# Performance work log

Hardware: AMD Instinct MI355X
Metric: run time of the kernel (lower is better)

## Reference

```python
import jax, jax.numpy as jnp
import numpy as np

N_CIRC, N_MIR, N_DIS = 100_000, 50_000, 25_000
IN_CH, HID, OUT = 128, 64, 64


def setup_inputs() -> dict:
    key = jax.random.key(0)
    ks = iter(jax.random.split(key, 64))

    def nrm(shape, scale):
        return jax.random.normal(next(ks), shape, jnp.float32) * scale

    def edges(n_src, n_dst, E):
        s = jax.random.randint(next(ks), (E,), 0, n_src, jnp.int32)
        d = jax.random.randint(next(ks), (E,), 0, n_dst, jnp.int32)
        return jnp.stack([s, d])  # [2, E]

    inp = dict(
        x_circ=nrm((N_CIRC, IN_CH), 1.0),
        x_mir=nrm((N_MIR, IN_CH), 1.0),
        x_dis=nrm((N_DIS, IN_CH), 1.0),
        e_cm=edges(N_CIRC, N_MIR, 500_000),
        e_md=edges(N_MIR, N_DIS, 250_000),
        e_cd=edges(N_CIRC, N_DIS, 250_000),
        e_mc=edges(N_MIR, N_CIRC, 500_000),
        e_dm=edges(N_DIS, N_MIR, 250_000),
        e_dc=edges(N_DIS, N_CIRC, 250_000),
        e_cc=edges(N_CIRC, N_CIRC, 500_000),
        e_mm=edges(N_MIR, N_MIR, 250_000),
        # stacked SAGEConv params: lin_l (with bias) and lin_r (no bias), per relation
        W1l=nrm((6, HID, IN_CH), 0.08), W1r=nrm((6, HID, IN_CH), 0.08), b1=jnp.zeros((6, HID), jnp.float32),
        W2l=nrm((6, HID, HID), 0.12), W2r=nrm((6, HID, HID), 0.12), b2=jnp.zeros((6, HID), jnp.float32),
        W3l=nrm((8, OUT, HID), 0.12), W3r=nrm((8, OUT, HID), 0.12), b3=jnp.zeros((8, OUT), jnp.float32),
    )
    return inp


def _sage(x_src, x_dst, ei, Wl, bl, Wr, n_dst):
    # PyG SAGEConv: out = lin_l(mean_j x_src[j]) + lin_r(x_dst); isolated dst -> 0 agg
    src, dst = ei[0], ei[1]
    msum = jax.ops.segment_sum(x_src[src], dst, num_segments=n_dst)
    cnt = jax.ops.segment_sum(jnp.ones(src.shape, x_src.dtype), dst, num_segments=n_dst)
    agg = msum / jnp.maximum(cnt, 1.0)[:, None]
    return agg @ Wl.T + bl + x_dst @ Wr.T


def _hetero_layer(xc, xm, xd, Wl, Wr, b, es, with_sim):
    e_cm, e_md, e_cd, e_mc, e_dm, e_dc, e_cc, e_mm = es
    o_cm = _sage(xc, xm, e_cm, Wl[0], b[0], Wr[0], N_MIR)
    o_md = _sage(xm, xd, e_md, Wl[1], b[1], Wr[1], N_DIS)
    o_cd = _sage(xc, xd, e_cd, Wl[2], b[2], Wr[2], N_DIS)
    o_mc = _sage(xm, xc, e_mc, Wl[3], b[3], Wr[3], N_CIRC)
    o_dm = _sage(xd, xm, e_dm, Wl[4], b[4], Wr[4], N_MIR)
    o_dc = _sage(xd, xc, e_dc, Wl[5], b[5], Wr[5], N_CIRC)
    if with_sim:
        o_cc = _sage(xc, xc, e_cc, Wl[6], b[6], Wr[6], N_CIRC)
        o_mm = _sage(xm, xm, e_mm, Wl[7], b[7], Wr[7], N_MIR)
        hc = (o_mc + o_dc + o_cc) / 3.0
        hm = (o_cm + o_dm + o_mm) / 3.0
    else:
        hc = (o_mc + o_dc) / 2.0
        hm = (o_cm + o_dm) / 2.0
    hd = (o_md + o_cd) / 2.0  # HeteroConv aggr='mean' across relations
    return hc, hm, hd


def _l2norm(x):
    n = jnp.sqrt(jnp.sum(x * x, axis=1, keepdims=True))
    return x / jnp.maximum(n, 1e-12)


def reference(x_circ, x_mir, x_dis, e_cm, e_md, e_cd, e_mc, e_dm, e_dc, e_cc, e_mm,
              W1l, W1r, b1, W2l, W2r, b2, W3l, W3r, b3):
    es = (e_cm, e_md, e_cd, e_mc, e_dm, e_dc, e_cc, e_mm)
    hc, hm, hd = _hetero_layer(x_circ, x_mir, x_dis, W1l, W1r, b1, es, False)
    hc, hm, hd = jax.nn.relu(hc), jax.nn.relu(hm), jax.nn.relu(hd)  # dropout = identity (eval)
    hc, hm, hd = _hetero_layer(hc, hm, hd, W2l, W2r, b2, es, False)
    hc, hm, hd = jax.nn.relu(hc), jax.nn.relu(hm), jax.nn.relu(hd)
    oc, om, od = _hetero_layer(hc, hm, hd, W3l, W3r, b3, es, True)
    return _l2norm(oc), _l2norm(om), _l2norm(od)
```

## Files before the change

### kernel.cpp

```cpp
#include <hip/hip_runtime.h>
#include <hip/hip_bf16.h>

#define DIV_UP(a,b) (((a)+(b)-1)/(b))

typedef __bf16 bf16x8 __attribute__((ext_vector_type(8)));
typedef float  f32x4  __attribute__((ext_vector_type(4)));

__global__ __launch_bounds__(256) void detect_dtype(const unsigned int* __restrict__ x,
                                                    int* __restrict__ flag) {
  __shared__ int cnt_s;
  if (threadIdx.x == 0) cnt_s = 0;
  __syncthreads();
  unsigned w = x[threadIdx.x];
  unsigned lo_exp = (w >> 7) & 0xFF;
  if (lo_exp >= 100 && lo_exp <= 140) atomicAdd(&cnt_s, 1);
  __syncthreads();
  if (threadIdx.x == 0) flag[0] = (cnt_s >= 128) ? 1 : 0;
}

template<int K>
__global__ __launch_bounds__(256) void gemm_mfma(
    const void* __restrict__ x, int xmode,
    const void* __restrict__ w, int woff, int wmode,
    const int* __restrict__ flagp, __hip_bfloat16* __restrict__ out, int n) {
  constexpr int KP = K + 8;
  __shared__ __bf16 xs[64 * KP];
  const bool xb = (xmode == 2) ? (*flagp != 0) : (xmode == 1);
  const bool wb = (wmode == 2) ? (*flagp != 0) : (wmode == 1);
  const int t = threadIdx.x;
  const int wv = t >> 6;
  const int L = t & 63;
  const int m = L & 15, q = L >> 4;
  const int row0 = blockIdx.x * 64;
  const int col = wv * 16 + m;

  bf16x8 bfr[K / 32];
  if (wb) {
    const __bf16* wh = (const __bf16*)w + woff;
#pragma unroll
    for (int ks = 0; ks < K / 32; ++ks)
      bfr[ks] = *(const bf16x8*)&wh[col * K + ks * 32 + q * 8];
  } else {
    const float* wf = (const float*)w + woff;
#pragma unroll
    for (int ks = 0; ks < K / 32; ++ks) {
      bf16x8 b;
#pragma unroll
      for (int j = 0; j < 8; ++j) b[j] = (__bf16)wf[col * K + ks * 32 + q * 8 + j];
      bfr[ks] = b;
    }
  }

  constexpr int CH = K / 8;
  if (xb) {
    const __bf16* xh = (const __bf16*)x;
    for (int idx = t; idx < 64 * CH; idx += 256) {
      int r = idx / CH, c = idx % CH;
      int gr = row0 + r; gr = (gr < n) ? gr : (n - 1);
      *(bf16x8*)&xs[r * KP + c * 8] = *(const bf16x8*)&xh[(size_t)gr * K + c * 8];
    }
  } else {
    const float* xf = (const float*)x;
    for (int idx = t; idx < 64 * CH; idx += 256) {
      int r = idx / CH, c = idx % CH;
      int gr = row0 + r; gr = (gr < n) ? gr : (n - 1);
      const float* src = &xf[(size_t)gr * K + c * 8];
      bf16x8 v;
#pragma unroll
      for (int j = 0; j < 8; ++j) v[j] = (__bf16)src[j];
      *(bf16x8*)&xs[r * KP + c * 8] = v;
    }
  }
  __syncthreads();

  f32x4 acc[4] = {};
#pragma unroll
  for (int ks = 0; ks < K / 32; ++ks) {
#pragma unroll
    for (int rt = 0; rt < 4; ++rt) {
      bf16x8 a = *(const bf16x8*)&xs[(rt * 16 + m) * KP + ks * 32 + q * 8];
      acc[rt] = __builtin_amdgcn_mfma_f32_16x16x32_bf16(a, bfr[ks], acc[rt], 0, 0, 0);
    }
  }

#pragma unroll
  for (int rt = 0; rt < 4; ++rt) {
#pragma unroll
    for (int i = 0; i < 4; ++i) {
      int gr = row0 + rt * 16 + q * 4 + i;
      if (gr < n) out[(size_t)gr * 64 + col] = __float2bfloat16(acc[rt][i]);
    }
  }
}

template<int K, int MODE, int NREL>
__global__ __launch_bounds__(256) void fused_agg(
    const void* __restrict__ xdst, int xmode,
    const int* __restrict__ flagp,
    const __hip_bfloat16* __restrict__ wrsum,
    const float* __restrict__ bias,
    const int* __restrict__ col,
    const int* __restrict__ rp0, const __hip_bfloat16* __restrict__ y0,
    const int* __restrict__ rp1, const __hip_bfloat16* __restrict__ y1,
    const int* __restrict__ rp2, const __hip_bfloat16* __restrict__ y2,
    float invR,
    void* __restrict__ outp, size_t obase, int n) {
  constexpr int CAP = 512;
  __shared__ float dbuf[16][68];
  __shared__ int rpl_s[NREL][17];
  __shared__ int cbuf[NREL][CAP];
  const bool xb = (xmode == 2) ? (*flagp != 0) : (xmode == 1);
  const int t = threadIdx.x;
  const int wv = t >> 6, L = t & 63;
  const int m = L & 15, q = L >> 4;
  const int row0 = blockIdx.x * 16;
  const int colc = wv * 16 + m;

  const int* rps[3] = {rp0, rp1, rp2};
  int hi16 = row0 + 16; hi16 = (hi16 < n) ? hi16 : n;
  int sj[NREL]; bool fit[NREL];
#pragma unroll
  for (int j = 0; j < NREL; ++j) {
    sj[j] = rps[j][row0];
    int span = rps[j][hi16] - sj[j];
    fit[j] = (span <= CAP);
    int lim = fit[j] ? span : 0;
    for (int i = t; i < lim; i += 256) cbuf[j][i] = col[sj[j] + i];
  }

  if (t < NREL * 17) {
    int j = t / 17, k = t - j * 17;
    const int* rp = (j == 0) ? rp0 : (j == 1) ? rp1 : rp2;
    int gi = row0 + k; gi = (gi < n) ? gi : n;
    rpl_s[j][k] = rp[gi];
  }

  const __bf16* wh = (const __bf16*)wrsum;
  bf16x8 bfr[K / 32];
#pragma unroll
  for (int ks = 0; ks < K / 32; ++ks)
    bfr[ks] = *(const bf16x8*)&wh[colc * K + ks * 32 + q * 8];

  int ar = row0 + m; ar = (ar < n) ? ar : (n - 1);
  f32x4 acc = {};
  if (xb) {
    const __bf16* xp = (const __bf16*)xdst;
#pragma unroll
    for (int ks = 0; ks < K / 32; ++ks) {
      bf16x8 a = *(const bf16x8*)&xp[(size_t)ar * K + ks * 32 + q * 8];
      acc = __builtin_amdgcn_mfma_f32_16x16x32_bf16(a, bfr[ks], acc, 0, 0, 0);
    }
  } else {
    const float* xp = (const float*)xdst;
#pragma unroll
    for (int ks = 0; ks < K / 32; ++ks) {
      bf16x8 a;
#pragma unroll
      for (int j = 0; j < 8; ++j) a[j] = (__bf16)xp[(size_t)ar * K + ks * 32 + q * 8 + j];
      acc = __builtin_amdgcn_mfma_f32_16x16x32_bf16(a, bfr[ks], acc, 0, 0, 0);
    }
  }
  float bc = bias[colc];
#pragma unroll
  for (int i = 0; i < 4; ++i) dbuf[q * 4 + i][colc] = acc[i] + bc;
  __syncthreads();

  const char* ys[3] = {(const char*)y0, (const char*)y1, (const char*)y2};
  const int jj = L & 31;
  const int half = L >> 5;
  const unsigned jb = (unsigned)jj << 2;

#pragma unroll 1
  for (int pass = 0; pass < 2; ++pass) {
    int b0[2][NREL], dg[2][NREL];
    float g0[2][NREL], g1[2][NREL];
    int nbmax = 0;
#pragma unroll
    for (int u = 0; u < 2; ++u) {
      const int lr = wv * 4 + pass * 2 + u;
#pragma unroll
      for (int j = 0; j < NREL; ++j) {
        int s = rpl_s[j][lr], e = rpl_s[j][lr + 1];
        b0[u][j] = s; dg[u][j] = e - s;
        g0[u][j] = 0.0f; g1[u][j] = 0.0f;
        int nbj = (e - s + 3) >> 2;
        nbmax = (nbj > nbmax) ? nbj : nbmax;
      }
    }

#pragma unroll 1
    for (int b = 0; b < nbmax; ++b) {
      const int bb = b << 2;
      unsigned wd[2][NREL][2];
#pragma unroll
      for (int u = 0; u < 2; ++u)
#pragma unroll
        for (int j = 0; j < NREL; ++j) {
          int rem = dg[u][j] - bb;
          if (rem > 0) {
            int last = rem - 1;
            int o0 = (half < last) ? half : last;
            int o1 = (2 + half < last) ? (2 + half) : last;
            unsigned c0, c1;
            if (fit[j]) {
              int lp = b0[u][j] - sj[j] + bb;
              c0 = (unsigned)cbuf[j][lp + o0];
              c1 = (unsigned)cbuf[j][lp + o1];
            } else {
              int p = b0[u][j] + bb;
              c0 = (unsigned)col[p + o0];
              c1 = (unsigned)col[p + o1];
            }
            wd[u][j][0] = *(const unsigned*)(ys[j] + ((c0 << 7) + jb));
            wd[u][j][1] = *(const unsigned*)(ys[j] + ((c1 << 7) + jb));
          }
        }
#pragma unroll
      for (int u = 0; u < 2; ++u)
#pragma unroll
        for (int j = 0; j < NREL; ++j) {
          int rem = dg[u][j] - bb;
          if (rem > 0) {
            unsigned w0 = (half < rem) ? wd[u][j][0] : 0u;
            unsigned w1 = (2 + half < rem) ? wd[u][j][1] : 0u;
            g0[u][j] += __uint_as_float(w0 << 16) + __uint_as_float(w1 << 16);
            g1[u][j] += __uint_as_float(w0 & 0xffff0000u) + __uint_as_float(w1 & 0xffff0000u);
          }
        }
    }

#pragma unroll
    for (int u = 0; u < 2; ++u) {
      const int lr = wv * 4 + pass * 2 + u;
      const int gr = row0 + lr;
      if (gr >= n) continue;
      float t0 = 0.0f, t1 = 0.0f;
#pragma unroll
      for (int j = 0; j < NREL; ++j) {
        float idg = (dg[u][j] > 0) ? (1.0f / (float)dg[u][j]) : 0.0f;
        t0 += g0[u][j] * idg; t1 += g1[u][j] * idg;
      }
      t0 += __shfl_xor(t0, 32, 64);
      t1 += __shfl_xor(t1, 32, 64);
      float2 d2 = *(const float2*)&dbuf[lr][2 * jj];
      float s0 = (d2.x + t0) * invR;
      float s1 = (d2.y + t1) * invR;

      if (MODE == 0) {
        if (half == 0) {
          __hip_bfloat16 b0v = __float2bfloat16(fmaxf(s0, 0.0f));
          __hip_bfloat16 b1v = __float2bfloat16(fmaxf(s1, 0.0f));
          unsigned pw = ((unsigned)*(const unsigned short*)&b1v << 16) |
                        (unsigned)*(const unsigned short*)&b0v;
          *(unsigned*)((__hip_bfloat16*)outp + obase + (size_t)gr * 64 + 2 * jj) = pw;
        }
      } else {
        float ss = s0 * s0 + s1 * s1;
#pragma unroll
        for (int o = 16; o > 0; o >>= 1) ss += __shfl_xor(ss, o, 64);
        float sc = 1.0f / fmaxf(sqrtf(ss), 1e-12f);
        float r0 = s0 * sc, r1 = s1 * sc;
        if (half == 0) {
          size_t idx = obase + (size_t)gr * 64 + 2 * jj;
          if (*flagp) {
            __hip_bfloat16 b0v = __float2bfloat16(r0);
            __hip_bfloat16 b1v = __float2bfloat16(r1);
            unsigned pw = ((unsigned)*(const unsigned short*)&b1v << 16) |
                          (unsigned)*(const unsigned short*)&b0v;
            *(unsigned*)((__hip_bfloat16*)outp + idx) = pw;
          } else {
            float2 v; v.x = r0; v.y = r1;
            *(float2*)((float*)outp + idx) = v;
          }
        }
      }
    }
  }
}

__global__ __launch_bounds__(256) void count_int(const int* __restrict__ ed,
                                                 int* __restrict__ deg, int E) {
  int i = blockIdx.x * 256 + threadIdx.x;
  if (i < E) atomicAdd(&deg[ed[i]], 1);
}

__global__ __launch_bounds__(256) void scan1(const int* __restrict__ deg,
    int* __restrict__ outp, int* __restrict__ part, int n) {
  __shared__ int tmp[256];
  int gid = blockIdx.x * 256 + threadIdx.x;
  int v = (gid < n) ? deg[gid] : 0;
  tmp[threadIdx.x] = v;
  __syncthreads();
  for (int off = 1; off < 256; off <<= 1) {
    int t = (threadIdx.x >= off) ? tmp[threadIdx.x - off] : 0;
    __syncthreads();
    tmp[threadIdx.x] += t;
    __syncthreads();
  }
  if (gid < n) outp[gid] = tmp[threadIdx.x] - v;
  if (threadIdx.x == 255) part[blockIdx.x] = tmp[255];
}

__global__ __launch_bounds__(256) void scan2(int* __restrict__ part, int P,
                                             int* __restrict__ totalout) {
  __shared__ int tmp[256];
  __shared__ int carry;
  if (threadIdx.x == 0) carry = 0;
  __syncthreads();
  for (int base0 = 0; base0 < P; base0 += 256) {
    int i = base0 + threadIdx.x;
    int v = (i < P) ? part[i] : 0;
    tmp[threadIdx.x] = v;
    __syncthreads();
    for (int off = 1; off < 256; off <<= 1) {
      int t = (threadIdx.x >= off) ? tmp[threadIdx.x - off] : 0;
      __syncthreads();
      tmp[threadIdx.x] += t;
      __syncthreads();
    }
    if (i < P) part[i] = tmp[threadIdx.x] - v + carry;
    __syncthreads();
    if (threadIdx.x == 0) carry += tmp[255];
    __syncthreads();
  }
  if (threadIdx.x == 0) *totalout = carry;
}

__global__ __launch_bounds__(256) void scan3(int* __restrict__ outp,
    const int* __restrict__ part, int n) {
  int gid = blockIdx.x * 256 + threadIdx.x;
  if (gid < n) outp[gid] += part[blockIdx.x];
}

__global__ __launch_bounds__(256) void copy_int(const int* __restrict__ src,
                                                int* __restrict__ dst, int n) {
  int i = blockIdx.x * 256 + threadIdx.x;
  if (i < n) dst[i] = src[i];
}

__global__ __launch_bounds__(256) void fill_csr(const int* __restrict__ es,
    const int* __restrict__ ed, int* __restrict__ cursor, int* __restrict__ col, int E) {
  int i = blockIdx.x * 256 + threadIdx.x;
  if (i < E) {
    int pos = atomicAdd(&cursor[ed[i]], 1);
    col[pos] = es[i];
  }
}

__global__ __launch_bounds__(256) void wsum_kernel(
    const void* __restrict__ W, int o0, int o1, int o2,
    const void* __restrict__ B, int p0, int p1, int p2,
    const int* __restrict__ flagp, __hip_bfloat16* __restrict__ wout,
    float* __restrict__ bout, int wsz) {
  const bool bf = (*flagp != 0);
  int i = blockIdx.x * 256 + threadIdx.x;
  float s = 0.0f, sb = 0.0f;
  if (bf) {
    const __hip_bfloat16* Wp = (const __hip_bfloat16*)W;
    const __hip_bfloat16* Bp = (const __hip_bfloat16*)B;
    if (i < wsz) {
      s = __bfloat162float(Wp[o0 + i]) + __bfloat162float(Wp[o1 + i]);
      if (o2 >= 0) s += __bfloat162float(Wp[o2 + i]);
    }
    if (i < 64) {
      sb = __bfloat162float(Bp[p0 + i]) + __bfloat162float(Bp[p1 + i]);
      if (p2 >= 0) sb += __bfloat162float(Bp[p2 + i]);
    }
  } else {
    const float* Wp = (const float*)W;
    const float* Bp = (const float*)B;
    if (i < wsz) {
      s = Wp[o0 + i] + Wp[o1 + i];
      if (o2 >= 0) s += Wp[o2 + i];
    }
    if (i < 64) {
      sb = Bp[p0 + i] + Bp[p1 + i];
      if (p2 >= 0) sb += Bp[p2 + i];
    }
  }
  if (i < wsz) wout[i] = __float2bfloat16(s);
  if (i < 64) bout[i] = sb;
}

extern "C" void kernel_launch(void* const* d_in, const int* in_sizes, int n_in,
                              void* d_out, int out_size, void* d_ws, size_t ws_size,
                              hipStream_t stream) {
  const int NC = 100000, NM = 50000, ND = 25000;
  const int nn[3] = {NC, NM, ND};
  const size_t toff[3] = {0, (size_t)NC * 64, (size_t)(NC + NM) * 64};
  const void* X[3] = {d_in[0], d_in[1], d_in[2]};
  const int* eptr[8]; int E[8];
  for (int r = 0; r < 8; ++r) { eptr[r] = (const int*)d_in[3 + r]; E[r] = in_sizes[3 + r] / 2; }
  const void* Wls[3] = {d_in[11], d_in[14], d_in[17]};
  const void* Wrs[3] = {d_in[12], d_in[15], d_in[18]};
  const void* Bbs[3] = {d_in[13], d_in[16], d_in[19]};

  const int src_t[8] = {0, 1, 0, 1, 2, 2, 0, 1};
  const int dst_t[8] = {1, 2, 2, 0, 1, 0, 0, 1};
  const int relT[3][3] = {{3, 5, 6}, {0, 4, 7}, {1, 2, -1}};

  int coff[8]; int cntN = 0;
  for (int r = 0; r < 8; ++r) { coff[r] = cntN; cntN += nn[dst_t[r]]; }
  int Etot = 0; for (int r = 0; r < 8; ++r) Etot += E[r];

  char* base = (char*)d_ws;
  auto carve = [&](size_t bytes) -> char* {
    char* p = (char*)(((uintptr_t)base + 127) & ~(uintptr_t)127);
    base = p + bytes;
    return p;
  };
  int* flag = (int*)carve(16);
  __hip_bfloat16* wr[3];
  for (int t = 0; t < 3; ++t) wr[t] = (__hip_bfloat16*)carve(64 * 128 * 2);
  float* bs[3]; for (int t = 0; t < 3; ++t) bs[t] = (float*)carve(64 * 4);
  __hip_bfloat16* y = (__hip_bfloat16*)carve((size_t)175000 * 64 * 2);
  int* degcur = (int*)carve((size_t)cntN * 4);
  int* rowptr = (int*)carve((size_t)(cntN + 1) * 4);
  int* part = (int*)carve((size_t)(DIV_UP(cntN, 256) + 1) * 4);
  int* col = (int*)carve((size_t)Etot * 4);
  __hip_bfloat16* h2 = (__hip_bfloat16*)carve((size_t)175000 * 64 * 2);
  __hip_bfloat16* h1 = (__hip_bfloat16*)d_out;
  (void)n_in; (void)out_size; (void)ws_size;

  detect_dtype<<<1, 256, 0, stream>>>((const unsigned int*)d_in[0], flag);

  hipMemsetAsync(degcur, 0, (size_t)cntN * sizeof(int), stream);
  for (int r = 0; r < 8; ++r)
    count_int<<<DIV_UP(E[r], 256), 256, 0, stream>>>(eptr[r] + E[r], degcur + coff[r], E[r]);
  int nb = DIV_UP(cntN, 256);
  scan1<<<nb, 256, 0, stream>>>(degcur, rowptr, part, cntN);
  scan2<<<1, 256, 0, stream>>>(part, nb, rowptr + cntN);
  scan3<<<nb, 256, 0, stream>>>(rowptr, part, cntN);
  copy_int<<<nb, 256, 0, stream>>>(rowptr, degcur, cntN);
  for (int r = 0; r < 8; ++r)
    fill_csr<<<DIV_UP(E[r], 256), 256, 0, stream>>>(eptr[r], eptr[r] + E[r],
                                                    degcur + coff[r], col, E[r]);

  for (int layer = 0; layer < 3; ++layer) {
    const void* Wl = Wls[layer];
    const void* Wr = Wrs[layer];
    const void* Bb = Bbs[layer];
    const int K = (layer == 0) ? 128 : 64;
    const int wsz = 64 * K;
    const __hip_bfloat16* hin = (layer == 1) ? h1 : h2;

    for (int T = 0; T < 3; ++T) {
      const int nrel = (layer == 2 && T < 2) ? 3 : 2;
      const int r0 = relT[T][0], r1 = relT[T][1];
      const int r2 = (nrel == 3) ? relT[T][2] : -1;
      wsum_kernel<<<DIV_UP(wsz, 256), 256, 0, stream>>>(
          Wr, r0 * wsz, r1 * wsz, (r2 >= 0) ? r2 * wsz : -1,
          Bb, r0 * 64, r1 * 64, (r2 >= 0) ? r2 * 64 : -1,
          flag, wr[T], bs[T], wsz);
      size_t yoffs[3] = {0, 0, 0};
      size_t yoff = 0;
      for (int j = 0; j < nrel; ++j) {
        int r = relT[T][j], st = src_t[r];
        yoffs[j] = yoff;
        if (layer == 0)
          gemm_mfma<128><<<DIV_UP(nn[st], 64), 256, 0, stream>>>(
              X[st], 2, Wl, r * wsz, 2, flag, y + yoff, nn[st]);
        else
          gemm_mfma<64><<<DIV_UP(nn[st], 64), 256, 0, stream>>>(
              hin + toff[st], 1, Wl, r * wsz, 2, flag, y + yoff, nn[st]);
        yoff += (size_t)nn[st] * 64;
      }
      const int* rp0 = rowptr + coff[r0];
      const int* rp1 = rowptr + coff[r1];
      const int* rp2 = (r2 >= 0) ? rowptr + coff[r2] : rp0;
      const __hip_bfloat16* y0 = y + yoffs[0];
      const __hip_bfloat16* y1 = y + yoffs[1];
      const __hip_bfloat16* y2 = (r2 >= 0) ? y + yoffs[2] : y0;
      int grid = DIV_UP(nn[T], 16);
      if (layer == 0) {
        fused_agg<128, 0, 2><<<grid, 256, 0, stream>>>(
            X[T], 2, flag, wr[T], bs[T], col, rp0, y0, rp1, y1, rp2, y2,
            0.5f, h1, toff[T], nn[T]);
      } else if (layer == 1) {
        fused_agg<64, 0, 2><<<grid, 256, 0, stream>>>(
            h1 + toff[T], 1, flag, wr[T], bs[T], col, rp0, y0, rp1, y1, rp2, y2,
            0.5f, h2, toff[T], nn[T]);
      } else if (T < 2) {
        fused_agg<64, 1, 3><<<grid, 256, 0, stream>>>(
            h2 + toff[T], 1, flag, wr[T], bs[T], col, rp0, y0, rp1, y1, rp2, y2,
            1.0f / 3.0f, d_out, toff[T], nn[T]);
      } else {
        fused_agg<64, 1, 2><<<grid, 256, 0, stream>>>(
            h2 + toff[T], 1, flag, wr[T], bs[T], col, rp0, y0, rp1, y1, rp2, y2,
            0.5f, d_out, toff[T], nn[T]);
      }
    }
  }
}
```

Measured before the change: 1.035 ms.

## Aggregate raw features before linear transform in layers 2 and 3

For the 64-wide layers, the per-relation GEMM that projected source features before gathering is removed. A new fused kernel gathers and mean-aggregates the raw hidden features per relation into shared memory, then applies W_l with MFMA alongside the W_r root term, bias, scaling, ReLU or L2-norm. This drops the intermediate y buffer writes and reads plus separate GEMM launches, and adds per-block MFMA work on the aggregated tile plus fp32-to-bf16 conversion of the aggregates. Layer 1 keeps the transform-then-aggregate path.

```diff
diff --git a/kernel.cpp b/kernel.cpp
--- a/kernel.cpp
+++ b/kernel.cpp
@@ -278,6 +278,210 @@
   }
 }
 
+template<int MODE, int NREL>
+__global__ __launch_bounds__(256) void fused_pre(
+    const __hip_bfloat16* __restrict__ xdst,
+    const int* __restrict__ flagp,
+    const void* __restrict__ Wl, int wo0, int wo1, int wo2,
+    const __hip_bfloat16* __restrict__ wrsum,
+    const float* __restrict__ bias,
+    const int* __restrict__ col,
+    const int* __restrict__ rp0, const __hip_bfloat16* __restrict__ hs0,
+    const int* __restrict__ rp1, const __hip_bfloat16* __restrict__ hs1,
+    const int* __restrict__ rp2, const __hip_bfloat16* __restrict__ hs2,
+    float invR, void* __restrict__ outp, size_t obase, int n) {
+  constexpr int K = 64, CAP = 256;
+  __shared__ float dbuf[16][68];
+  __shared__ float abuf[NREL][16][68];
+  __shared__ int rpl_s[NREL][17];
+  __shared__ int cbuf[NREL][CAP];
+  const bool wb = (*flagp != 0);
+  const int t = threadIdx.x;
+  const int wv = t >> 6, L = t & 63;
+  const int m = L & 15, q = L >> 4;
+  const int row0 = blockIdx.x * 16;
+  const int colc = wv * 16 + m;
+
+  const int* rps[3] = {rp0, rp1, rp2};
+  int hi16 = row0 + 16; hi16 = (hi16 < n) ? hi16 : n;
+  int sj[NREL]; bool fit[NREL];
+#pragma unroll
+  for (int j = 0; j < NREL; ++j) {
+    sj[j] = rps[j][row0];
+    int span = rps[j][hi16] - sj[j];
+    fit[j] = (span <= CAP);
+    int lim = fit[j] ? span : 0;
+    for (int i = t; i < lim; i += 256) cbuf[j][i] = col[sj[j] + i];
+  }
+  if (t < NREL * 17) {
+    int j = t / 17, k = t - j * 17;
+    const int* rp = (j == 0) ? rp0 : (j == 1) ? rp1 : rp2;
+    int gi = row0 + k; gi = (gi < n) ? gi : n;
+    rpl_s[j][k] = rp[gi];
+  }
+
+  const __bf16* wh = (const __bf16*)wrsum;
+  int ar = row0 + m; ar = (ar < n) ? ar : (n - 1);
+  f32x4 acc = {};
+  {
+    const __bf16* xp = (const __bf16*)xdst;
+#pragma unroll
+    for (int ks = 0; ks < 2; ++ks) {
+      bf16x8 bw = *(const bf16x8*)&wh[colc * K + ks * 32 + q * 8];
+      bf16x8 a = *(const bf16x8*)&xp[(size_t)ar * K + ks * 32 + q * 8];
+      acc = __builtin_amdgcn_mfma_f32_16x16x32_bf16(a, bw, acc, 0, 0, 0);
+    }
+  }
+  __syncthreads();
+
+  const char* hsb[3] = {(const char*)hs0, (const char*)hs1, (const char*)hs2};
+  const int jj = L & 31;
+  const int half = L >> 5;
+  const unsigned jb = (unsigned)jj << 2;
+
+#pragma unroll 1
+  for (int pass = 0; pass < 2; ++pass) {
+    int b0[2][NREL], dg[2][NREL];
+    float g0[2][NREL], g1[2][NREL];
+    int nbmax = 0;
+#pragma unroll
+    for (int u = 0; u < 2; ++u) {
+      const int lr = wv * 4 + pass * 2 + u;
+#pragma unroll
+      for (int j = 0; j < NREL; ++j) {
+        int s = rpl_s[j][lr], e = rpl_s[j][lr + 1];
+        b0[u][j] = s; dg[u][j] = e - s;
+        g0[u][j] = 0.0f; g1[u][j] = 0.0f;
+        int nbj = (e - s + 3) >> 2;
+        nbmax = (nbj > nbmax) ? nbj : nbmax;
+      }
+    }
+
+#pragma unroll 1
+    for (int b = 0; b < nbmax; ++b) {
+      const int bb = b << 2;
+      unsigned wd[2][NREL][2];
+#pragma unroll
+      for (int u = 0; u < 2; ++u)
+#pragma unroll
+        for (int j = 0; j < NREL; ++j) {
+          int rem = dg[u][j] - bb;
+          if (rem > 0) {
+            int last = rem - 1;
+            int o0 = (half < last) ? half : last;
+            int o1 = (2 + half < last) ? (2 + half) : last;
+            unsigned c0, c1;
+            if (fit[j]) {
+              int lp = b0[u][j] - sj[j] + bb;
+              c0 = (unsigned)cbuf[j][lp + o0];
+              c1 = (unsigned)cbuf[j][lp + o1];
+            } else {
+              int p = b0[u][j] + bb;
+              c0 = (unsigned)col[p + o0];
+              c1 = (unsigned)col[p + o1];
+            }
+            wd[u][j][0] = *(const unsigned*)(hsb[j] + ((c0 << 7) + jb));
+            wd[u][j][1] = *(const unsigned*)(hsb[j] + ((c1 << 7) + jb));
+          }
+        }
+#pragma unroll
+      for (int u = 0; u < 2; ++u)
+#pragma unroll
+        for (int j = 0; j < NREL; ++j) {
+          int rem = dg[u][j] - bb;
+          if (rem > 0) {
+            unsigned w0 = (half < rem) ? wd[u][j][0] : 0u;
+            unsigned w1 = (2 + half < rem) ? wd[u][j][1] : 0u;
+            g0[u][j] += __uint_as_float(w0 << 16) + __uint_as_float(w1 << 16);
+            g1[u][j] += __uint_as_float(w0 & 0xffff0000u) + __uint_as_float(w1 & 0xffff0000u);
+          }
+        }
+    }
+
+#pragma unroll
+    for (int u = 0; u < 2; ++u) {
+      const int lr = wv * 4 + pass * 2 + u;
+#pragma unroll
+      for (int j = 0; j < NREL; ++j) {
+        float idg = (dg[u][j] > 0) ? (1.0f / (float)dg[u][j]) : 0.0f;
+        float t0 = g0[u][j] * idg, t1 = g1[u][j] * idg;
+        t0 += __shfl_xor(t0, 32, 64);
+        t1 += __shfl_xor(t1, 32, 64);
+        if (half == 0) {
+          abuf[j][lr][2 * jj] = t0;
+          abuf[j][lr][2 * jj + 1] = t1;
+        }
+      }
+    }
+  }
+  __syncthreads();
+
+  const int wos[3] = {wo0, wo1, wo2};
+#pragma unroll
+  for (int j = 0; j < NREL; ++j) {
+#pragma unroll
+    for (int ks = 0; ks < 2; ++ks) {
+      bf16x8 bw;
+      if (wb) {
+        const __bf16* p = (const __bf16*)Wl + wos[j];
+        bw = *(const bf16x8*)&p[colc * K + ks * 32 + q * 8];
+      } else {
+        const float* p = (const float*)Wl + wos[j];
+#pragma unroll
+        for (int e = 0; e < 8; ++e) bw[e] = (__bf16)p[colc * K + ks * 32 + q * 8 + e];
+      }
+      const float* arow = &abuf[j][m][ks * 32 + q * 8];
+      bf16x8 ba;
+#pragma unroll
+      for (int e = 0; e < 8; ++e) ba[e] = (__bf16)arow[e];
+      acc = __builtin_amdgcn_mfma_f32_16x16x32_bf16(ba, bw, acc, 0, 0, 0);
+    }
+  }
+
+  float bc = bias[colc];
+#pragma unroll
+  for (int i = 0; i < 4; ++i) dbuf[q * 4 + i][colc] = acc[i] + bc;
+  __syncthreads();
+
+#pragma unroll
+  for (int rr = 0; rr < 4; ++rr) {
+    const int lr = wv * 4 + rr;
+    const int gr = row0 + lr;
+    if (gr >= n) continue;
+    float2 d2 = *(const float2*)&dbuf[lr][2 * jj];
+    float s0 = d2.x * invR;
+    float s1 = d2.y * invR;
+    if (MODE == 0) {
+      if (half == 0) {
+        __hip_bfloat16 b0v = __float2bfloat16(fmaxf(s0, 0.0f));
+        __hip_bfloat16 b1v = __float2bfloat16(fmaxf(s1, 0.0f));
+        unsigned pw = ((unsigned)*(const unsigned short*)&b1v << 16) |
+                      (unsigned)*(const unsigned short*)&b0v;
+        *(unsigned*)((__hip_bfloat16*)outp + obase + (size_t)gr * 64 + 2 * jj) = pw;
+      }
+    } else {
+      float ss = s0 * s0 + s1 * s1;
+#pragma unroll
+      for (int o = 16; o > 0; o >>= 1) ss += __shfl_xor(ss, o, 64);
+      float sc = 1.0f / fmaxf(sqrtf(ss), 1e-12f);
+      float r0 = s0 * sc, r1 = s1 * sc;
+      if (half == 0) {
+        size_t idx = obase + (size_t)gr * 64 + 2 * jj;
+        if (*flagp) {
+          __hip_bfloat16 b0v = __float2bfloat16(r0);
+          __hip_bfloat16 b1v = __float2bfloat16(r1);
+          unsigned pw = ((unsigned)*(const unsigned short*)&b1v << 16) |
+                        (unsigned)*(const unsigned short*)&b0v;
+          *(unsigned*)((__hip_bfloat16*)outp + idx) = pw;
+        } else {
+          float2 v; v.x = r0; v.y = r1;
+          *(float2*)((float*)outp + idx) = v;
+        }
+      }
+    }
+  }
+}
+
 __global__ __launch_bounds__(256) void count_int(const int* __restrict__ ed,
                                                  int* __restrict__ deg, int E) {
   int i = blockIdx.x * 256 + threadIdx.x;
@@ -436,12 +640,39 @@
     fill_csr<<<DIV_UP(E[r], 256), 256, 0, stream>>>(eptr[r], eptr[r] + E[r],
                                                     degcur + coff[r], col, E[r]);
 
-  for (int layer = 0; layer < 3; ++layer) {
+  {
+    const void* Wl = Wls[0];
+    const void* Wr = Wrs[0];
+    const void* Bb = Bbs[0];
+    const int wsz = 64 * 128;
+    for (int T = 0; T < 3; ++T) {
+      const int r0 = relT[T][0], r1 = relT[T][1];
+      wsum_kernel<<<DIV_UP(wsz, 256), 256, 0, stream>>>(
+          Wr, r0 * wsz, r1 * wsz, -1, Bb, r0 * 64, r1 * 64, -1,
+          flag, wr[T], bs[T], wsz);
+      size_t yoffs[2] = {0, 0};
+      size_t yoff = 0;
+      for (int j = 0; j < 2; ++j) {
+        int r = relT[T][j], st = src_t[r];
+        yoffs[j] = yoff;
+        gemm_mfma<128><<<DIV_UP(nn[st], 64), 256, 0, stream>>>(
+            X[st], 2, Wl, r * wsz, 2, flag, y + yoff, nn[st]);
+        yoff += (size_t)nn[st] * 64;
+      }
+      const int* rp0 = rowptr + coff[r0];
+      const int* rp1 = rowptr + coff[r1];
+      int grid = DIV_UP(nn[T], 16);
+      fused_agg<128, 0, 2><<<grid, 256, 0, stream>>>(
+          X[T], 2, flag, wr[T], bs[T], col, rp0, y + yoffs[0], rp1, y + yoffs[1],
+          rp0, y + yoffs[0], 0.5f, h1, toff[T], nn[T]);
+    }
+  }
+
+  for (int layer = 1; layer < 3; ++layer) {
     const void* Wl = Wls[layer];
     const void* Wr = Wrs[layer];
     const void* Bb = Bbs[layer];
-    const int K = (layer == 0) ? 128 : 64;
-    const int wsz = 64 * K;
+    const int wsz = 64 * 64;
     const __hip_bfloat16* hin = (layer == 1) ? h1 : h2;
 
     for (int T = 0; T < 3; ++T) {
@@ -452,41 +683,27 @@
           Wr, r0 * wsz, r1 * wsz, (r2 >= 0) ? r2 * wsz : -1,
           Bb, r0 * 64, r1 * 64, (r2 >= 0) ? r2 * 64 : -1,
           flag, wr[T], bs[T], wsz);
-      size_t yoffs[3] = {0, 0, 0};
-      size_t yoff = 0;
-      for (int j = 0; j < nrel; ++j) {
-        int r = relT[T][j], st = src_t[r];
-        yoffs[j] = yoff;
-        if (layer == 0)
-          gemm_mfma<128><<<DIV_UP(nn[st], 64), 256, 0, stream>>>(
-              X[st], 2, Wl, r * wsz, 2, flag, y + yoff, nn[st]);
-        else
-          gemm_mfma<64><<<DIV_UP(nn[st], 64), 256, 0, stream>>>(
-              hin + toff[st], 1, Wl, r * wsz, 2, flag, y + yoff, nn[st]);
-        yoff += (size_t)nn[st] * 64;
-      }
       const int* rp0 = rowptr + coff[r0];
       const int* rp1 = rowptr + coff[r1];
       const int* rp2 = (r2 >= 0) ? rowptr + coff[r2] : rp0;
-      const __hip_bfloat16* y0 = y + yoffs[0];
-      const __hip_bfloat16* y1 = y + yoffs[1];
-      const __hip_bfloat16* y2 = (r2 >= 0) ? y + yoffs[2] : y0;
+      const __hip_bfloat16* g0p = hin + toff[src_t[r0]];
+      const __hip_bfloat16* g1p = hin + toff[src_t[r1]];
+      const __hip_bfloat16* g2p = (r2 >= 0) ? hin + toff[src_t[r2]] : g0p;
       int grid = DIV_UP(nn[T], 16);
-      if (layer == 0) {
-        fused_agg<128, 0, 2><<<grid, 256, 0, stream>>>(
-            X[T], 2, flag, wr[T], bs[T], col, rp0, y0, rp1, y1, rp2, y2,
-            0.5f, h1, toff[T], nn[T]);
-      } else if (layer == 1) {
-        fused_agg<64, 0, 2><<<grid, 256, 0, stream>>>(
-            h1 + toff[T], 1, flag, wr[T], bs[T], col, rp0, y0, rp1, y1, rp2, y2,
+      if (layer == 1) {
+        fused_pre<0, 2><<<grid, 256, 0, stream>>>(
+            hin + toff[T], flag, Wl, r0 * wsz, r1 * wsz, -1,
+            wr[T], bs[T], col, rp0, g0p, rp1, g1p, rp0, g0p,
             0.5f, h2, toff[T], nn[T]);
       } else if (T < 2) {
-        fused_agg<64, 1, 3><<<grid, 256, 0, stream>>>(
-            h2 + toff[T], 1, flag, wr[T], bs[T], col, rp0, y0, rp1, y1, rp2, y2,
+        fused_pre<1, 3><<<grid, 256, 0, stream>>>(
+            hin + toff[T], flag, Wl, r0 * wsz, r1 * wsz, r2 * wsz,
+            wr[T], bs[T], col, rp0, g0p, rp1, g1p, rp2, g2p,
             1.0f / 3.0f, d_out, toff[T], nn[T]);
       } else {
-        fused_agg<64, 1, 2><<<grid, 256, 0, stream>>>(
-            h2 + toff[T], 1, flag, wr[T], bs[T], col, rp0, y0, rp1, y1, rp2, y2,
+        fused_pre<1, 2><<<grid, 256, 0, stream>>>(
+            hin + toff[T], flag, Wl, r0 * wsz, r1 * wsz, -1,
+            wr[T], bs[T], col, rp0, g0p, rp1, g1p, rp0, g0p,
             0.5f, d_out, toff[T], nn[T]);
       }
     }
```

Result: no change. 1.053 ms (+1.7%).
